# Kernel tuning notes

Measured on AMD Instinct MI355X. Metric: run time of the kernel, lower is better.

## Reference

```python
import jax, jax.numpy as jnp
import numpy as np

B, L, F, H, HDE, E, V, MH, MW, TOUT = 64, 2, 512, 512, 512, 512, 94, 6, 40, 30
V2 = V + 2          # vocab + START/END + NULL slots
T = TOUT + 2        # decode steps
HW = MH * MW
START = V + 1
END = V + 1


def setup_inputs() -> dict:
    key = jax.random.key(0)
    ks = jax.random.split(key, 20)
    s = 0.05  # weight scale for numerical stability
    n = lambda k, shape: jax.random.normal(k, shape, jnp.float32) * s
    d = {}
    d['conv_f'] = jax.random.normal(ks[0], (B, F, MH, MW), jnp.float32)
    d['target'] = jax.random.randint(ks[1], (B, TOUT), 0, 95, dtype=jnp.int32)
    d['w_ih_en'] = n(ks[2], (L, 4 * H, F))
    d['w_hh_en'] = n(ks[3], (L, 4 * H, H))
    d['b_ih_en'] = n(ks[4], (L, 4 * H))
    d['b_hh_en'] = n(ks[5], (L, 4 * H))
    d['embed_w'] = n(ks[6], (V2, H))
    d['w_ih_de'] = n(ks[7], (L, 4 * HDE, H))
    d['w_hh_de'] = n(ks[8], (L, 4 * HDE, HDE))
    d['b_ih_de'] = n(ks[9], (L, 4 * HDE))
    d['b_hh_de'] = n(ks[10], (L, 4 * HDE))
    d['att_wh'] = n(ks[11], (E, HDE))
    d['att_bh'] = n(ks[12], (E,))
    d['att_conv_w'] = n(ks[13], (E, F, 3, 3))
    d['att_conv_b'] = n(ks[14], (E,))
    d['att_wv'] = n(ks[15], (1, E))
    d['att_bv'] = n(ks[16], (1,))
    d['out_w'] = n(ks[17], (V2, HDE + F))
    d['out_b'] = n(ks[18], (V2,))
    return d


def _lstm_cell(x, h, c, wih, whh, bih, bhh):
    # PyTorch gate order: i, f, g, o
    g = x @ wih.T + h @ whh.T + bih + bhh
    i, f, gg, o = jnp.split(g, 4, axis=-1)
    c_new = jax.nn.sigmoid(f) * c + jax.nn.sigmoid(i) * jnp.tanh(gg)
    h_new = jax.nn.sigmoid(o) * jnp.tanh(c_new)
    return h_new, c_new


def _forward(conv_f, target, w_ih_en, w_hh_en, b_ih_en, b_hh_en, embed_w,
             w_ih_de, w_hh_de, b_ih_de, b_hh_de, att_wh, att_bh,
             att_conv_w, att_conv_b, att_wv, att_bv, out_w, out_b):
    # ---- encoder: maxpool over full height, then 2-layer LSTM over width ----
    x_seq = jnp.max(conv_f, axis=2).transpose(2, 0, 1)  # [W, B, F]

    def enc_step(carry, xt):
        h, c = carry
        inp = xt
        hs, cs = [], []
        for l in range(L):
            hl, cl = _lstm_cell(inp, h[l], c[l], w_ih_en[l], w_hh_en[l],
                                b_ih_en[l], b_hh_en[l])
            inp = hl
            hs.append(hl); cs.append(cl)
        return (jnp.stack(hs), jnp.stack(cs)), inp

    z = jnp.zeros((L, B, H), conv_f.dtype)
    _, enc_out = jax.lax.scan(enc_step, (z, z), x_seq)
    holistic = enc_out[-1]  # [B, H]

    # ---- attention: conv_f embedding computed ONCE (invariant across steps) ----
    xe = jax.lax.conv_general_dilated(
        conv_f, att_conv_w, (1, 1), 'SAME',
        dimension_numbers=('NCHW', 'OIHW', 'NCHW')) + att_conv_b[None, :, None, None]
    x_em = xe.reshape(B, E, HW).transpose(0, 2, 1)       # [B, HW, E]
    cf_flat = conv_f.reshape(B, F, HW).transpose(0, 2, 1)  # [B, HW, F]

    # ---- decoder inputs: t=0 holistic, t>=1 embed(gt_with_start[:, t-1]) ----
    gt = jnp.concatenate(
        [jnp.full((B, 1), START, dtype=target.dtype), target], axis=1)  # [B, T-1]
    xs = jnp.concatenate([holistic[None], embed_w[gt.T]], axis=0)  # [T, B, H]

    def dec_step(carry, xt):
        h, c = carry
        inp = xt
        hs, cs = [], []
        for l in range(L):
            hl, cl = _lstm_cell(inp, h[l], c[l], w_ih_de[l], w_hh_de[l],
                                b_ih_de[l], b_hh_de[l])
            inp = hl
            hs.append(hl); cs.append(cl)
        hlast = inp  # [B, HDE]
        g_em = hlast @ att_wh.T + att_bh                    # [B, E]
        feat = jnp.tanh(x_em + g_em[:, None, :])            # [B, HW, E] (dropout=identity)
        e = feat @ att_wv[0] + att_bv[0]                    # [B, HW]
        alpha = jax.nn.softmax(e, axis=-1)
        att = jnp.einsum('bw,bwf->bf', alpha, cf_flat)      # [B, F]
        logits = jnp.concatenate([hlast, att], axis=-1) @ out_w.T + out_b
        scores = jax.nn.log_softmax(logits, axis=-1)        # [B, V2]
        return (jnp.stack(hs), jnp.stack(cs)), scores

    zd = jnp.zeros((B, HDE), conv_f.dtype)
    z0 = jnp.stack([zd] * L)
    _, out_tbv = jax.lax.scan(dec_step, (z0, z0), xs)  # [T, B, V2]
    out = out_tbv.transpose(1, 0, 2)                    # [B, T, V2]

    # ---- build l_target: [0, target..., 0] with first padding 0 -> END ----
    l_target = jnp.zeros((B, T), jnp.int32).at[:, 1:-1].set(target)
    j = jnp.argmax(l_target[:, 1:] == 0, axis=1) + 1  # first zero at col>=1 (always exists)
    l_target = l_target.at[jnp.arange(B), j].set(END)

    # ---- masked NLL loss ----
    lt = l_target.reshape(-1)
    nll = -out.reshape(-1, V2)[jnp.arange(B * T), lt]
    mask = (lt != 0).astype(out.dtype)
    return jnp.sum(nll * mask) / jnp.sum(mask)


def reference(conv_f, target, w_ih_en, w_hh_en, b_ih_en, b_hh_en, embed_w,
              w_ih_de, w_hh_de, b_ih_de, b_hh_de, att_wh, att_bh,
              att_conv_w, att_conv_b, att_wv, att_bv, out_w, out_b):
    return _forward(conv_f, target, w_ih_en, w_hh_en, b_ih_en, b_hh_en, embed_w,
                    w_ih_de, w_hh_de, b_ih_de, b_hh_de, att_wh, att_bh,
                    att_conv_w, att_conv_b, att_wv, att_bv, out_w, out_b)
```

## Files before the change

kernel.cpp:

```cpp
#include <hip/hip_runtime.h>

typedef __fp16 f16;
typedef __fp16 f16x4 __attribute__((ext_vector_type(4)));
typedef __fp16 f16x8 __attribute__((ext_vector_type(8)));
typedef float  f32x4 __attribute__((ext_vector_type(4)));
typedef unsigned long long ull;

#define DEV static __device__ __forceinline__

DEV f32x4 mfma16(f16x4 a, f16x4 b, f32x4 c) {
  return __builtin_amdgcn_mfma_f32_16x16x16f16(a, b, c, 0, 0, 0);
}
DEV f16x4 lo4(f16x8 v) { return __builtin_shufflevector(v, v, 0, 1, 2, 3); }
DEV f16x4 hi4(f16x8 v) { return __builtin_shufflevector(v, v, 4, 5, 6, 7); }
DEV float sigf(float x) { return 1.f / (1.f + __expf(-x)); }
DEV float tanh_(float x) { float e = __expf(2.f * x); return 1.f - 2.f / (e + 1.f); }

union U8 { float4 f4; float2 f2[2]; };
union H2 { unsigned u; f16 h[2]; };
union H4 { ull u; f16 h[4]; f16x4 v; };

#define HB 32768

DEV ull ldU(const ull* p) {
  return __hip_atomic_load(p, __ATOMIC_RELAXED, __HIP_MEMORY_SCOPE_AGENT);
}
DEV unsigned ldF(const unsigned* p) {
  return __hip_atomic_load(p, __ATOMIC_RELAXED, __HIP_MEMORY_SCOPE_AGENT);
}
DEV void stU32(unsigned* p, unsigned v) {
  __hip_atomic_store(p, v, __ATOMIC_RELAXED, __HIP_MEMORY_SCOPE_AGENT);
}
DEV void stU64(ull* p, ull v) {
  __hip_atomic_store(p, v, __ATOMIC_RELAXED, __HIP_MEMORY_SCOPE_AGENT);
}

DEV void wait8(const unsigned* line, unsigned tgt) {
  if (threadIdx.x < 8)
    while (ldF(line + threadIdx.x * 16) < tgt) {}
  __syncthreads();
}

DEV void signalDone(unsigned* line, int slot) {
  asm volatile("s_waitcnt vmcnt(0)" ::: "memory");
  __syncthreads();
  if (threadIdx.x == 0)
    __hip_atomic_fetch_add(line + slot * 16, 1u, __ATOMIC_RELAXED, __HIP_MEMORY_SCOPE_AGENT);
}

DEV void stageRow(const f16* __restrict__ s, f16* __restrict__ dstRow, int ch) {
  U8 u0, u1;
  u0.f4 = *(const float4*)s;
  u1.f4 = *(const float4*)(s + 8);
  *(float2*)(dstRow +  0 + ch * 4) = u0.f2[0];
  *(float2*)(dstRow + 16 + ch * 4) = u0.f2[1];
  *(float2*)(dstRow + 32 + ch * 4) = u1.f2[0];
  *(float2*)(dstRow + 48 + ch * 4) = u1.f2[1];
}

DEV void stageAu(const ull* __restrict__ srcU, f16 (*A)[64][72], int tid) {
  int row = tid >> 2, ch = tid & 3;
  const ull* s = srcU + row * 128 + ch * 4;
#pragma unroll
  for (int c = 0; c < 8; ++c) {
    ull d0 = ldU(s + c * 16 + 0);
    ull d1 = ldU(s + c * 16 + 1);
    ull d2 = ldU(s + c * 16 + 2);
    ull d3 = ldU(s + c * 16 + 3);
    f16* d = &A[c][row][0];
    *(ull*)(d +  0 + ch * 4) = d0;
    *(ull*)(d + 16 + ch * 4) = d1;
    *(ull*)(d + 32 + ch * 4) = d2;
    *(ull*)(d + 48 + ch * 4) = d3;
  }
}

DEV void kloop32(const f16 (*Wt)[32][72], const f16 (*A)[64][72],
                 int mh, int ns, int m16, int g4, f32x4 acc[2]) {
#pragma unroll
  for (int c = 0; c < 8; ++c) {
#pragma unroll
    for (int half = 0; half < 2; ++half) {
      f16x8 bf = *(const f16x8*)&Wt[c][ns * 16 + m16][g4 * 16 + half * 8];
      f16x4 bl = lo4(bf), bh = hi4(bf);
#pragma unroll
      for (int mt = 0; mt < 2; ++mt) {
        f16x8 af = *(const f16x8*)&A[c][mh * 32 + mt * 16 + m16][g4 * 16 + half * 8];
        acc[mt] = mfma16(lo4(af), bl, acc[mt]);
        acc[mt] = mfma16(hi4(af), bh, acc[mt]);
      }
// ... 51 lines not shown
        } else {
          float2 z = make_float2(0.f, 0.f);
          *(float2*)&At[t][ 0] = z; *(float2*)&At[t][ 8] = z;
          *(float2*)&At[t][16] = z; *(float2*)&At[t][24] = z;
          *(float2*)&At[t][ 4] = z; *(float2*)&At[t][12] = z;
          *(float2*)&At[t][20] = z; *(float2*)&At[t][28] = z;
        }
      }
      {
        int n = t >> 1, ch = t & 1;
        const f16* s = wc9 + (size_t)(eb + n) * 4608 + kr * 512 + f0 + ch * 16;
        U8 u0, u1;
        u0.f4 = *(const float4*)s; u1.f4 = *(const float4*)(s + 8);
        *(float2*)&Bt[n][ 0 + ch * 4] = u0.f2[0];
        *(float2*)&Bt[n][ 8 + ch * 4] = u0.f2[1];
        *(float2*)&Bt[n][16 + ch * 4] = u1.f2[0];
        *(float2*)&Bt[n][24 + ch * 4] = u1.f2[1];
      }
      __syncthreads();
      f16x8 b0 = *(const f16x8*)&Bt[w * 32 + m16][g4 * 8];
      f16x8 b1v = *(const f16x8*)&Bt[w * 32 + 16 + m16][g4 * 8];
      f16x4 b0l = lo4(b0), b0h = hi4(b0), b1l = lo4(b1v), b1h = hi4(b1v);
#pragma unroll
      for (int mt = 0; mt < 15; ++mt) {
        f16x8 af = *(const f16x8*)&At[mt * 16 + m16][g4 * 8];
        f16x4 al = lo4(af), ah = hi4(af);
        acc[mt][0] = mfma16(al, b0l, acc[mt][0]);
        acc[mt][1] = mfma16(al, b1l, acc[mt][1]);
        acc[mt][0] = mfma16(ah, b0h, acc[mt][0]);
        acc[mt][1] = mfma16(ah, b1h, acc[mt][1]);
      }
    }
  }
#pragma unroll
  for (int nt = 0; nt < 2; ++nt) {
    int e = eb + w * 32 + nt * 16 + m16;
    float bias = cb[e];
#pragma unroll
    for (int mt = 0; mt < 15; ++mt)
#pragma unroll
      for (int r = 0; r < 4; ++r) {
        int p = mt * 16 + g4 * 4 + r;
        xemH[((size_t)(b * 240 + p)) * 512 + e] = (f16)(acc[mt][nt][r] + bias);
      }
  }
}


__global__ void k_convW(const float* __restrict__ s0, const float* __restrict__ s1,
                        const float* __restrict__ s2, const float* __restrict__ s3,
                        f16* __restrict__ d0, f16* __restrict__ d1,
                        f16* __restrict__ d2, f16* __restrict__ d3) {
  int i = blockIdx.x * 256 + threadIdx.x;
  int sel = i >> 19, j = i & 524287;
  const float* s = sel == 0 ? s0 : sel == 1 ? s1 : sel == 2 ? s2 : s3;
  f16* d = sel == 0 ? d0 : sel == 1 ? d1 : sel == 2 ? d2 : d3;
  float4 v = ((const float4*)s)[j];
  f16x4 o = { (f16)v.x, (f16)v.y, (f16)v.z, (f16)v.w };
  *(f16x4*)(d + (size_t)j * 4) = o;
}

__global__ void k_convS(const float* __restrict__ awhS, const float* __restrict__ embS,
                        const float* __restrict__ outwS,
                        f16* __restrict__ awhD, f16* __restrict__ embD,
                        f16* __restrict__ outwD) {
  int i = blockIdx.x * 256 + threadIdx.x;
  const float* s; f16* d; int j;
  if (i < 65536) { s = awhS; d = awhD; j = i; }
  else if (i < 65536 + 12288) { s = embS; d = embD; j = i - 65536; }
  else if (i < 65536 + 12288 + 24576) { s = outwS; d = outwD; j = i - 65536 - 12288; }
  else return;
  float4 v = ((const float4*)s)[j];
  f16x4 o = { (f16)v.x, (f16)v.y, (f16)v.z, (f16)v.w };
  *(f16x4*)(d + (size_t)j * 4) = o;
}

__global__ __launch_bounds__(256) void k_wc9(const float* __restrict__ src, f16* __restrict__ dst) {
// ... 18 lines not shown
    float4 v = ((const float4*)src)[i];
    int fl = i / 60, pc = (i % 60) * 4;
    sT[fl][pc] = v.x; sT[fl][pc + 1] = v.y; sT[fl][pc + 2] = v.z; sT[fl][pc + 3] = v.w;
  }
  __syncthreads();
  if (tid < 240) {
    int p = tid;
    f16* drow = cfT + ((size_t)b * 240 + p) * 512 + f0;
#pragma unroll
    for (int j = 0; j < 8; ++j) {
      f16x8 o;
#pragma unroll
      for (int k = 0; k < 8; ++k) o[k] = (f16)sT[j * 8 + k][p];
      *(f16x8*)(drow + j * 8) = o;
    }
  }
  {
    int fl = tid >> 2, wq = tid & 3;
#pragma unroll
    for (int wi = 0; wi < 10; ++wi) {
      int w = wq * 10 + wi;
      float m = sT[fl][w];
#pragma unroll
      for (int h = 1; h < 6; ++h) m = fmaxf(m, sT[fl][h * 40 + w]);
      xseq[((size_t)w * 64 + b) * 512 + f0 + fl] = (f16)m;
    }
  }
}

__global__ void k_zero(unsigned* p0, unsigned* p1, unsigned* p2,
                       unsigned* p3, unsigned* p4, unsigned* p5) {
  int i = blockIdx.x * 256 + threadIdx.x;
  int sel = i >> 14, j = i & 16383;
  unsigned* p = sel == 0 ? p0 : sel == 1 ? p1 : sel == 2 ? p2 :
                sel == 3 ? p3 : sel == 4 ? p4 : p5;
  p[j] = 0;
}

__global__ __launch_bounds__(256) void k_gemmX(
    const f16* __restrict__ A, const f16* __restrict__ W,
    const float* __restrict__ b1, const float* __restrict__ b2,
    f16* __restrict__ C)
{
  __shared__ f16 At[64][72];
  __shared__ f16 Bt[64][72];
  const int t = threadIdx.x, lane = t & 63, g = t >> 6;
  f32x4 acc[4] = {};
  const int m16 = lane & 15, g4 = lane >> 4;
  const size_t arow0 = (size_t)blockIdx.x * 64;

  for (int k0 = 0; k0 < 512; k0 += 64) {
    __syncthreads();
    { int row = t >> 2, ch = t & 3;
      stageRow(A + (arow0 + row) * 512 + k0 + ch * 16, &At[row][0], ch); }
    { int row = t >> 2, ch = t & 3;
      stageRow(W + ((size_t)blockIdx.y * 64 + row) * 512 + k0 + ch * 16, &Bt[row][0], ch); }
    __syncthreads();
#pragma unroll
    for (int half = 0; half < 2; ++half) {
      f16x8 bf = *(const f16x8*)&Bt[g * 16 + m16][g4 * 16 + half * 8];
      f16x4 bl = lo4(bf), bh = hi4(bf);
#pragma unroll
      for (int mt = 0; mt < 4; ++mt) {
        f16x8 af = *(const f16x8*)&At[mt * 16 + m16][g4 * 16 + half * 8];
        acc[mt] = mfma16(lo4(af), bl, acc[mt]);
        acc[mt] = mfma16(hi4(af), bh, acc[mt]);
      }
    }
// ... 21 lines not shown
  const size_t arow0 = (size_t)tt * 64;
  const int row = t >> 2, ch = t & 3;
  const f16* rowSrc;
  if (tt == 0) rowSrc = x_t0 + (size_t)row * 512;
  else if (tt == 1) rowSrc = emb + (size_t)95 * 512;
  else { int tok = tgt[row * 30 + tt - 2]; rowSrc = emb + (size_t)tok * 512; }

  for (int k0 = 0; k0 < 512; k0 += 64) {
    __syncthreads();
    stageRow(rowSrc + k0 + ch * 16, &At[row][0], ch);
    stageRow(W + ((size_t)blockIdx.y * 64 + row) * 512 + k0 + ch * 16, &Bt[row][0], ch);
    __syncthreads();
#pragma unroll
    for (int half = 0; half < 2; ++half) {
      f16x8 bf = *(const f16x8*)&Bt[g * 16 + m16][g4 * 16 + half * 8];
      f16x4 bl = lo4(bf), bh = hi4(bf);
#pragma unroll
      for (int mt = 0; mt < 4; ++mt) {
        f16x8 af = *(const f16x8*)&At[mt * 16 + m16][g4 * 16 + half * 8];
        acc[mt] = mfma16(lo4(af), bl, acc[mt]);
        acc[mt] = mfma16(hi4(af), bh, acc[mt]);
      }
    }
  }
  int e = blockIdx.y * 64 + g * 16 + m16;
  float bias = b1[e] + b2[e];
#pragma unroll
  for (int mt = 0; mt < 4; ++mt)
#pragma unroll
    for (int r = 0; r < 4; ++r)
      C[(arow0 + mt * 16 + g4 * 4 + r) * 2048 + e] = (f16)(acc[mt][r] + bias);
}

__global__ __launch_bounds__(256) void k_gemmG(
    const f16* __restrict__ A, const f16* __restrict__ W,
    const float* __restrict__ b1, f16* __restrict__ C)
{
  __shared__ f16 At[64][72];
  __shared__ f16 Bt[64][72];
  const int t = threadIdx.x, lane = t & 63, g = t >> 6;
  f32x4 acc[4] = {};
  const int m16 = lane & 15, g4 = lane >> 4;
  const size_t arow0 = (size_t)blockIdx.x * 64;

  for (int k0 = 0; k0 < 512; k0 += 64) {
    __syncthreads();
    { int row = t >> 2, ch = t & 3;
      stageRow(A + (arow0 + row) * 512 + k0 + ch * 16, &At[row][0], ch); }
    { int row = t >> 2, ch = t & 3;
      stageRow(W + ((size_t)blockIdx.y * 64 + row) * 512 + k0 + ch * 16, &Bt[row][0], ch); }
    __syncthreads();
#pragma unroll
    for (int half = 0; half < 2; ++half) {
      f16x8 bf = *(const f16x8*)&Bt[g * 16 + m16][g4 * 16 + half * 8];
      f16x4 bl = lo4(bf), bh = hi4(bf);
#pragma unroll
      for (int mt = 0; mt < 4; ++mt) {
        f16x8 af = *(const f16x8*)&At[mt * 16 + m16][g4 * 16 + half * 8];
        acc[mt] = mfma16(lo4(af), bl, acc[mt]);
        acc[mt] = mfma16(hi4(af), bh, acc[mt]);
      }
    }
  }
  int e = blockIdx.y * 64 + g * 16 + m16;
  float bias = b1[e];
#pragma unroll
  for (int mt = 0; mt < 4; ++mt)
#pragma unroll
    for (int r = 0; r < 4; ++r)
      C[(arow0 + mt * 16 + g4 * 4 + r) * 512 + e] = (f16)(acc[mt][r] + bias);
}

__global__ __launch_bounds__(256, 1) void k_lstm(
    int T,
    const f16* __restrict__ G0, const f16* __restrict__ whh0,
    const f16* __restrict__ wih1, const f16* __restrict__ whh1,
    const float* __restrict__ bih1, const float* __restrict__ bhh1,
    f16* __restrict__ h0seq, f16* __restrict__ h1seq,
    unsigned* __restrict__ cnt,
    const f16* __restrict__ cfT, const f16* __restrict__ wc9,
    const float* __restrict__ cb, f16* __restrict__ xemH, int convBase)
{
  __shared__ __align__(16) char smem[147456];
  const int tid = threadIdx.x, lane = tid & 63, w = tid >> 6;
  const int m16 = lane & 15, g4 = lane >> 4;
  const int bid = blockIdx.x;

  if (bid >= 96) {
    convTile(smem, convBase + bid - 96, cfT, wc9, cb, xemH);
    return;
  }

  if (bid < 32) {
    f16 (*sW)[64][72] = (f16(*)[64][72])smem;
    f16 (*sA)[64][72] = (f16(*)[64][72])(smem + 73728);
    float* sG = (float*)(smem + 73728);
    const int utile = bid;
    { int r = tid >> 2, ch = tid & 3;
      int grow = (r >> 4) * 512 + utile * 16 + (r & 15);
      for (int c = 0; c < 8; ++c)
        stageRow(whh0 + (size_t)grow * 512 + c * 64 + ch * 16, &sW[c][r][0], ch);
    }
    const int pb = tid >> 2, uq = tid & 3;
    float cst[4] = {0.f, 0.f, 0.f, 0.f};
    for (int t = 0; t < T; ++t) {
      if (t > 0) wait8(cnt + (size_t)(t - 1) * 128, 4);
      const f16* gpp = G0 + (size_t)(t * 64 + pb) * 2048 + utile * 16 + uq * 4;
      H4 gI, gF, gG, gO;
      gI.v = *(const f16x4*)(gpp);
      gF.v = *(const f16x4*)(gpp + 512);
      gG.v = *(const f16x4*)(gpp + 1024);
      gO.v = *(const f16x4*)(gpp + 1536);
      stageAu((const ull*)h0seq + (size_t)t * 8192, sA, tid);
      __syncthreads();
      f32x4 acc[4] = {};
      kloop64((const f16*)sW, sA, w, m16, g4, acc);
      __syncthreads();
#pragma unroll
      for (int mt = 0; mt < 4; ++mt)
#pragma unroll
        for (int r = 0; r < 4; ++r)
          sG[((size_t)w * 64 + mt * 16 + g4 * 4 + r) * 17 + m16] = acc[mt][r];
      __syncthreads();
      {
        H4 outp;
#pragma unroll
        for (int j = 0; j < 4; ++j) {
          int u = uq * 4 + j;
          float gi = sG[(0 * 64 + pb) * 17 + u] + (float)gI.h[j];
          float gf = sG[(1 * 64 + pb) * 17 + u] + (float)gF.h[j];
          float gg = sG[(2 * 64 + pb) * 17 + u] + (float)gG.h[j];
          float go = sG[(3 * 64 + pb) * 17 + u] + (float)gO.h[j];
          float cn = sigf(gf) * cst[j] + sigf(gi) * tanh_(gg);
          float hn = sigf(go) * tanh_(cn);
          cst[j] = cn;
          outp.h[j] = (f16)hn;
        }
        stU64((ull*)h0seq + (size_t)(t + 1) * 8192 + pb * 128 + utile * 4 + uq, outp.u);
      }
      signalDone(cnt + (size_t)t * 128, bid & 7);
    }
  } else {
    f16 (*sW2)[8][32][72] = (f16(*)[8][32][72])smem;
    f16 (*sA)[64][72] = (f16(*)[64][72])(smem + 73728);
    float* sG = (float*)(smem + 73728);
    const int utile = bid - 32;
    const int mh = w >> 1, ns = w & 1;
    { int mat = tid >> 7;
      int r = (tid >> 2) & 31, ch = tid & 3;
      int grow = (r >> 3) * 512 + utile * 8 + (r & 7);
      const f16* Wsrc = (mat == 0) ? wih1 : whh1;
      for (int c = 0; c < 8; ++c)
        stageRow(Wsrc + (size_t)grow * 512 + c * 64 + ch * 16, &sW2[mat][c][r][0], ch);
    }
    const int pb = tid >> 2, pup = tid & 3;
    float badd[4][2];
#pragma unroll
    for (int g = 0; g < 4; ++g)
#pragma unroll
      for (int j = 0; j < 2; ++j) {
        int rr = g * 512 + utile * 8 + pup * 2 + j;
        badd[g][j] = bih1[rr] + bhh1[rr];
      }
    float cst[2] = {0.f, 0.f};
    unsigned* line1 = cnt + (size_t)T * 128;
    for (int t = 0; t < T; ++t) {
      wait8(cnt + (size_t)t * 128, 4);
      stageAu((const ull*)h0seq + (size_t)(t + 1) * 8192, sA, tid);
      if (t > 0) wait8(line1 + (size_t)(t - 1) * 128, 8);
      else       __syncthreads();
      ull rg[8][4];
      { const ull* s1p = (const ull*)h1seq + (size_t)t * 8192 + (tid >> 2) * 128 + (tid & 3) * 4;
#pragma unroll
        for (int c = 0; c < 8; ++c)
#pragma unroll
// ... 13 lines not shown
        }
      }
      __syncthreads();
      kloop32(sW2[1], sA, mh, ns, m16, g4, acc);
      __syncthreads();
      { int nl = ns * 16 + m16;
#pragma unroll
        for (int mt = 0; mt < 2; ++mt)
#pragma unroll
          for (int r = 0; r < 4; ++r) {
            int b = mh * 32 + mt * 16 + g4 * 4 + r;
            sG[((nl >> 3) * 64 + b) * 9 + (nl & 7)] = acc[mt][r];
          }
      }
      __syncthreads();
      {
        H2 outp;
#pragma unroll
        for (int j = 0; j < 2; ++j) {
          int u = pup * 2 + j;
          float gi = sG[(0 * 64 + pb) * 9 + u] + badd[0][j];
          float gf = sG[(1 * 64 + pb) * 9 + u] + badd[1][j];
          float gg = sG[(2 * 64 + pb) * 9 + u] + badd[2][j];
          float go = sG[(3 * 64 + pb) * 9 + u] + badd[3][j];
          float cn = sigf(gf) * cst[j] + sigf(gi) * tanh_(gg);
          float hn = sigf(go) * tanh_(cn);
          cst[j] = cn;
          outp.h[j] = (f16)hn;
        }
        stU32((unsigned*)h1seq + (size_t)(t + 1) * 16384 + pb * 256 + utile * 4 + pup, outp.u);
      }
      signalDone(line1 + (size_t)t * 128, bid & 7);
    }
  }
}


__global__ __launch_bounds__(256) void k_scoreAll(
    const f16* __restrict__ xemH, const f16* __restrict__ gAll,
    const float* __restrict__ wv, float* __restrict__ esc)
{
  __shared__ f16 sX[20][512];
  const int tid = threadIdx.x, lane = tid & 63, w = tid >> 6;
  const int tile = blockIdx.x, b = blockIdx.y;
  for (int i = tid; i < 20 * 64; i += 256) {
    int row = i >> 6, seg = i & 63;
    *(f16x8*)&sX[row][seg * 8] =
        *(const f16x8*)(xemH + ((size_t)(b * 240 + tile * 20 + row)) * 512 + seg * 8);
  }
  float w8[8];
  { const float4* wp = (const float4*)(wv + lane * 8);
    float4 wa = wp[0], wb = wp[1];
    w8[0] = wa.x; w8[1] = wa.y; w8[2] = wa.z; w8[3] = wa.w;
    w8[4] = wb.x; w8[5] = wb.y; w8[6] = wb.z; w8[7] = wb.w; }
  __syncthreads();
  for (int t = 0; t < 32; ++t) {
    f16x8 gv = *(const f16x8*)(gAll + ((size_t)(t * 64 + b)) * 512 + lane * 8);
    float g8[8];
#pragma unroll
    for (int j = 0; j < 8; ++j) g8[j] = (float)gv[j];
#pragma unroll
    for (int i = 0; i < 5; ++i) {
      int rr = i * 4 + w;
      f16x8 xv = *(const f16x8*)&sX[rr][lane * 8];
      float s = 0.f;
#pragma unroll
      for (int j = 0; j < 8; ++j) s += tanh_((float)xv[j] + g8[j]) * w8[j];
#pragma unroll
      for (int m = 32; m; m >>= 1) s += __shfl_xor(s, m);
      if (lane == 0) esc[((size_t)(t * 64 + b)) * 240 + tile * 20 + rr] = s;
    }
  }
}

__global__ __launch_bounds__(256) void k_smctx(
    const float* __restrict__ esc, const f16* __restrict__ cfT,
    const f16* __restrict__ h1seq, f16* __restrict__ ctx)
{
  __shared__ float aAl[8][240];
  const int tid = threadIdx.x, lane = tid & 63, w = tid >> 6;
  const int tq = blockIdx.x, b = blockIdx.y;
  for (int half = 0; half < 2; ++half) {
    int tt = w + half * 4;
    int t = tq * 8 + tt;
    const float* er = esc + ((size_t)(t * 64 + b)) * 240;
    float v[4];
    float mx = -1e30f;
#pragma unroll
    for (int q = 0; q < 4; ++q) {
      int p = lane + q * 64;
      v[q] = (p < 240) ? er[p] : -1e30f;
      mx = fmaxf(mx, v[q]);
    }
#pragma unroll
    for (int m = 32; m; m >>= 1) mx = fmaxf(mx, __shfl_xor(mx, m));
    float sum = 0.f;
#pragma unroll
    for (int q = 0; q < 4; ++q) { v[q] = __expf(v[q] - mx); sum += v[q]; }
#pragma unroll
    for (int m = 32; m; m >>= 1) sum += __shfl_xor(sum, m);
    float inv = 1.f / sum;
#pragma unroll
    for (int q = 0; q < 4; ++q) {
      int p = lane + q * 64;
      if (p < 240) aAl[tt][p] = v[q] * inv;
    }
  }
  __syncthreads();
  float acc[8][2] = {};
  const f16* cb = cfT + (size_t)b * 240 * 512;
  for (int p = 0; p < 240; ++p) {
    H2 cw; cw.u = *(const unsigned*)(cb + (size_t)p * 512 + tid * 2);
    float c0 = (float)cw.h[0], c1 = (float)cw.h[1];
#pragma unroll
    for (int tt = 0; tt < 8; ++tt) {
      float a = aAl[tt][p];
      acc[tt][0] += a * c0;
      acc[tt][1] += a * c1;
    }
  }
#pragma unroll
  for (int tt = 0; tt < 8; ++tt) {
    int t = tq * 8 + tt;
    size_t r = (size_t)(t * 64 + b);
    H2 o; o.h[0] = (f16)acc[tt][0]; o.h[1] = (f16)acc[tt][1];
    *(unsigned*)(ctx + r * 1024 + 512 + tid * 2) = o.u;
    *(unsigned*)(ctx + r * 1024 + tid * 2) =
        *(const unsigned*)(h1seq + (size_t)(t + 1) * HB + b * 512 + tid * 2);
  }
}

__global__ __launch_bounds__(256) void k_gemmL(
    const f16* __restrict__ A, const f16* __restrict__ W,
    const float* __restrict__ bias, float* __restrict__ C)
{
  __shared__ f16 At[64][72];
  __shared__ f16 Bt[64][72];
  const int t = threadIdx.x, lane = t & 63, g = t >> 6;
  f32x4 acc[4] = {};
  const int m16 = lane & 15, g4 = lane >> 4;
  const size_t arow0 = (size_t)blockIdx.x * 64;

  for (int k0 = 0; k0 < 1024; k0 += 64) {
    __syncthreads();
    { int row = t >> 2, ch = t & 3;
      stageRow(A + (arow0 + row) * 1024 + k0 + ch * 16, &At[row][0], ch); }
    { int row = t >> 2, ch = t & 3;
      stageRow(W + ((size_t)(blockIdx.y * 64 + row)) * 1024 + k0 + ch * 16, &Bt[row][0], ch); }
    __syncthreads();
#pragma unroll
    for (int half = 0; half < 2; ++half) {
      f16x8 bf = *(const f16x8*)&Bt[g * 16 + m16][g4 * 16 + half * 8];
      f16x4 bl = lo4(bf), bh = hi4(bf);
#pragma unroll
      for (int mt = 0; mt < 4; ++mt) {
        f16x8 af = *(const f16x8*)&At[mt * 16 + m16][g4 * 16 + half * 8];
        acc[mt] = mfma16(lo4(af), bl, acc[mt]);
        acc[mt] = mfma16(hi4(af), bh, acc[mt]);
      }
    }
  }
  int e = blockIdx.y * 64 + g * 16 + m16;
  if (e < 96) {
    float be = bias[e];
#pragma unroll
    for (int mt = 0; mt < 4; ++mt)
#pragma unroll
      for (int r = 0; r < 4; ++r)
        C[(arow0 + mt * 16 + g4 * 4 + r) * 96 + e] = acc[mt][r] + be;
  }
}

__global__ void k_nllloss(const float* __restrict__ lgt, const int* __restrict__ target,
                          float* __restrict__ out) {
  __shared__ int ltg[2048];
  __shared__ float sa[256], sb[256];
  int tid = threadIdx.x;
  if (tid < 64) {
    int b = tid;
    int row[32];
    row[0] = 0;
    for (int t = 1; t <= 30; ++t) row[t] = target[b * 30 + t - 1];
    row[31] = 0;
    int j = 1;
    while (row[j] != 0) ++j;
    row[j] = 95;
    for (int t = 0; t < 32; ++t) ltg[b * 32 + t] = row[t];
  }
  __syncthreads();
  float a = 0.f, m = 0.f;
  for (int r = tid; r < 2048; r += 256) {
    int t = r >> 6, b = r & 63;
    int tok = ltg[b * 32 + t];
    if (tok != 0) {
      const float* row = lgt + (size_t)r * 96;
      float mx = -1e30f;
      for (int j = 0; j < 96; ++j) mx = fmaxf(mx, row[j]);
      float s = 0.f;
      for (int j = 0; j < 96; ++j) s += __expf(row[j] - mx);
      a += mx + __logf(s) - row[tok];
      m += 1.f;
    }
  }
  sa[tid] = a; sb[tid] = m; __syncthreads();
  for (int s = 128; s; s >>= 1) { if (tid < s) { sa[tid] += sa[tid + s]; sb[tid] += sb[tid + s]; } __syncthreads(); }
  if (tid == 0) out[0] = sa[0] / sb[0];
}


extern "C" void kernel_launch(void* const* d_in, const int* in_sizes, int n_in,
                              void* d_out, int out_size, void* d_ws, size_t ws_size,
                              hipStream_t stream) {
  (void)in_sizes; (void)n_in; (void)out_size; (void)ws_size;
  const float* conv_f = (const float*)d_in[0];
  const int*   target = (const int*)d_in[1];
  const float* wih_en = (const float*)d_in[2];
  const float* whh_en = (const float*)d_in[3];
  const float* bih_en = (const float*)d_in[4];
  const float* bhh_en = (const float*)d_in[5];
  const float* embed  = (const float*)d_in[6];
  const float* wih_de = (const float*)d_in[7];
  const float* whh_de = (const float*)d_in[8];
  const float* bih_de = (const float*)d_in[9];
  const float* bhh_de = (const float*)d_in[10];
  const float* att_wh = (const float*)d_in[11];
  const float* att_bh = (const float*)d_in[12];
  const float* att_cw = (const float*)d_in[13];
  const float* att_cb = (const float*)d_in[14];
  const float* att_wv = (const float*)d_in[15];
  const float* out_w  = (const float*)d_in[17];
  const float* out_b  = (const float*)d_in[18];
  float* out = (float*)d_out;

  size_t o = 0;
  char* base = (char*)d_ws;
  auto take = [&](size_t bytes) -> void* {
    void* p = base + o;
    o += (bytes + 255) & ~(size_t)255;
    return p;
  };
  const size_t WSZ = (size_t)2048 * 512;
  f16* wihEn = (f16*)take(2 * WSZ * 2);
  f16* whhEn = (f16*)take(2 * WSZ * 2);
  f16* wihDe = (f16*)take(2 * WSZ * 2);
  f16* whhDe = (f16*)take(2 * WSZ * 2);
  f16* awh   = (f16*)take((size_t)512 * 512 * 2);
  f16* emb   = (f16*)take((size_t)96 * 512 * 2);
  f16* wc9   = (f16*)take((size_t)512 * 4608 * 2);
  f16* cfT   = (f16*)take((size_t)64 * 240 * 512 * 2);
  f16* xseq  = (f16*)take((size_t)40 * 64 * 512 * 2);
  f16* xemH  = (f16*)take((size_t)64 * 240 * 512 * 2);
  f16* outwH = (f16*)take((size_t)128 * 1024 * 2);
  f16* X0en  = (f16*)take((size_t)2560 * 2048 * 2);
  f16* X0de  = (f16*)take((size_t)2048 * 2048 * 2);
  f16* h0seqE = (f16*)take((size_t)41 * HB * 2);
  f16* h1seqE = (f16*)take((size_t)41 * HB * 2);
  f16* h0seqD = (f16*)take((size_t)33 * HB * 2);
  f16* h1seqD = (f16*)take((size_t)33 * HB * 2);
  f16* gAll   = (f16*)take((size_t)2048 * 512 * 2);
  unsigned* cntE = (unsigned*)take(65536);
  unsigned* cntD = (unsigned*)take(65536);
  float* escAll = (float*)X0en;
  float* lgtAll = (float*)((char*)X0en + 4194304);
  f16*   ctxAll = X0de;

  k_convW<<<8192, 256, 0, stream>>>(wih_en, whh_en, wih_de, whh_de,
                                    wihEn, whhEn, wihDe, whhDe);
  k_convS<<<400, 256, 0, stream>>>(att_wh, embed, out_w, awh, emb, outwH);
  k_wc9<<<512, 256, 0, stream>>>(att_cw, wc9);
  k_cfmx<<<dim3(8, 64), 256, 0, stream>>>(conv_f, cfT, xseq);
  k_zero<<<384, 256, 0, stream>>>((unsigned*)h0seqE, (unsigned*)h1seqE,
                                  (unsigned*)h0seqD, (unsigned*)h1seqD, cntE, cntD);

  k_gemmX<<<dim3(40, 32), 256, 0, stream>>>(xseq, wihEn, bih_en, bhh_en, X0en);
  k_lstm<<<224, 256, 0, stream>>>(40, X0en, whhEn, wihEn + WSZ, whhEn + WSZ,
                                  bih_en + 2048, bhh_en + 2048, h0seqE, h1seqE, cntE,
                                  cfT, wc9, att_cb, xemH, 0);

  k_gemmXd<<<dim3(32, 32), 256, 0, stream>>>(h1seqE + (size_t)40 * HB, emb, target,
                                             wihDe, bih_de, bhh_de, X0de);
  k_lstm<<<224, 256, 0, stream>>>(32, X0de, whhDe, wihDe + WSZ, whhDe + WSZ,
                                  bih_de + 2048, bhh_de + 2048, h0seqD, h1seqD, cntD,
                                  cfT, wc9, att_cb, xemH, 128);

  k_gemmG<<<dim3(32, 8), 256, 0, stream>>>(h1seqD + HB, awh, att_bh, gAll);
  k_scoreAll<<<dim3(12, 64), 256, 0, stream>>>(xemH, gAll, att_wv, escAll);
  k_smctx<<<dim3(4, 64), 256, 0, stream>>>(escAll, cfT, h1seqD, ctxAll);
  k_gemmL<<<dim3(32, 2), 256, 0, stream>>>(ctxAll, outwH, out_b, lgtAll);
  k_nllloss<<<1, 256, 0, stream>>>(lgtAll, target, out);
}
```

Measured before the change: 856.4 us.

## Fuse attention, logits and NLL tail into persistent LSTM kernel with flag pipelining

The post-decoder stages (attention-query GEMM, score computation, softmax-context, logit GEMM, per-token NLL) move into the idle conv blocks of the decoder LSTM kernel. They are chained by counter flags so they overlap with the recurrence instead of running as separate launches. The embedding part of the decoder input GEMM is computed by extra blocks during the encoder LSTM, leaving only the t=0 row for k_gemmXd. The conv tile output is staged through LDS for coalesced atomic stores. The cost is more spin-waiting, atomic-load traffic and scratch buffers, and a risk of deadlock if the blocks are not all co-resident.

```diff
diff --git a/kernel.cpp b/kernel.cpp
--- a/kernel.cpp
+++ b/kernel.cpp
@@ -19,6 +19,7 @@
 union U8 { float4 f4; float2 f2[2]; };
 union H2 { unsigned u; f16 h[2]; };
 union H4 { ull u; f16 h[4]; f16x4 v; };
+union U32F { unsigned u; float f; };
 
 #define HB 32768
 
@@ -35,11 +36,12 @@
   __hip_atomic_store(p, v, __ATOMIC_RELAXED, __HIP_MEMORY_SCOPE_AGENT);
 }
 
-DEV void wait8(const unsigned* line, unsigned tgt) {
-  if (threadIdx.x < 8)
+DEV void waitN(const unsigned* line, int n, unsigned tgt) {
+  if ((int)threadIdx.x < n)
     while (ldF(line + threadIdx.x * 16) < tgt) {}
   __syncthreads();
 }
+DEV void wait8(const unsigned* line, unsigned tgt) { waitN(line, 8, tgt); }
 
 DEV void signalDone(unsigned* line, int slot) {
   asm volatile("s_waitcnt vmcnt(0)" ::: "memory");
@@ -56,6 +58,14 @@
   *(float2*)(dstRow + 16 + ch * 4) = u0.f2[1];
   *(float2*)(dstRow + 32 + ch * 4) = u1.f2[0];
   *(float2*)(dstRow + 48 + ch * 4) = u1.f2[1];
+}
+
+DEV void stageAp(const f16* __restrict__ rowSrc, f16 (*A)[64][72], int tid) {
+  int ch = tid & 3;
+  const f16* s = rowSrc + ch * 16;
+#pragma unroll
+  for (int c = 0; c < 8; ++c)
+    stageRow(s + c * 64, &A[c][tid >> 2][0], ch);
 }
 
 DEV void stageAu(const ull* __restrict__ srcU, f16 (*A)[64][72], int tid) {
@@ -173,6 +183,8 @@
       }
     }
   }
+  f16 (*sC)[132] = (f16(*)[132])smem;
+  __syncthreads();
 #pragma unroll
   for (int nt = 0; nt < 2; ++nt) {
     int e = eb + w * 32 + nt * 16 + m16;
@@ -180,10 +192,16 @@
 #pragma unroll
     for (int mt = 0; mt < 15; ++mt)
 #pragma unroll
-      for (int r = 0; r < 4; ++r) {
-        int p = mt * 16 + g4 * 4 + r;
-        xemH[((size_t)(b * 240 + p)) * 512 + e] = (f16)(acc[mt][nt][r] + bias);
-      }
+      for (int r = 0; r < 4; ++r)
+        sC[mt * 16 + g4 * 4 + r][w * 32 + nt * 16 + m16] = (f16)(acc[mt][nt][r] + bias);
+  }
+  __syncthreads();
+#pragma unroll
+  for (int k = 0; k < 30; ++k) {
+    int id = t + k * 256;
+    int row = id >> 5, chk = id & 31;
+    H4 pk; pk.v = *(const f16x4*)&sC[row][chk * 4];
+    stU64((ull*)xemH + (size_t)(b * 240 + row) * 128 + (eb >> 2) + chk, pk.u);
   }
 }
 
@@ -268,8 +286,13 @@
                        unsigned* p3, unsigned* p4, unsigned* p5) {
   int i = blockIdx.x * 256 + threadIdx.x;
   int sel = i >> 14, j = i & 16383;
-  unsigned* p = sel == 0 ? p0 : sel == 1 ? p1 : sel == 2 ? p2 :
-                sel == 3 ? p3 : sel == 4 ? p4 : p5;
+  unsigned* p;
+  if (sel == 0) p = p0;
+  else if (sel == 1) p = p1;
+  else if (sel == 2) p = p2;
+  else if (sel == 3) p = p3;
+  else if (sel == 4) p = p4;
+  else p = p5 + (size_t)(sel - 5) * 16384;
   p[j] = 0;
 }
 
@@ -357,64 +380,27 @@
       C[(arow0 + mt * 16 + g4 * 4 + r) * 2048 + e] = (f16)(acc[mt][r] + bias);
 }
 
-__global__ __launch_bounds__(256) void k_gemmG(
-    const f16* __restrict__ A, const f16* __restrict__ W,
-    const float* __restrict__ b1, f16* __restrict__ C)
-{
-  __shared__ f16 At[64][72];
-  __shared__ f16 Bt[64][72];
-  const int t = threadIdx.x, lane = t & 63, g = t >> 6;
-  f32x4 acc[4] = {};
-  const int m16 = lane & 15, g4 = lane >> 4;
-  const size_t arow0 = (size_t)blockIdx.x * 64;
-
-  for (int k0 = 0; k0 < 512; k0 += 64) {
-    __syncthreads();
-    { int row = t >> 2, ch = t & 3;
-      stageRow(A + (arow0 + row) * 512 + k0 + ch * 16, &At[row][0], ch); }
-    { int row = t >> 2, ch = t & 3;
-      stageRow(W + ((size_t)blockIdx.y * 64 + row) * 512 + k0 + ch * 16, &Bt[row][0], ch); }
-    __syncthreads();
-#pragma unroll
-    for (int half = 0; half < 2; ++half) {
-      f16x8 bf = *(const f16x8*)&Bt[g * 16 + m16][g4 * 16 + half * 8];
-      f16x4 bl = lo4(bf), bh = hi4(bf);
-#pragma unroll
-      for (int mt = 0; mt < 4; ++mt) {
-        f16x8 af = *(const f16x8*)&At[mt * 16 + m16][g4 * 16 + half * 8];
-        acc[mt] = mfma16(lo4(af), bl, acc[mt]);
-        acc[mt] = mfma16(hi4(af), bh, acc[mt]);
-      }
-    }
-  }
-  int e = blockIdx.y * 64 + g * 16 + m16;
-  float bias = b1[e];
-#pragma unroll
-  for (int mt = 0; mt < 4; ++mt)
-#pragma unroll
-    for (int r = 0; r < 4; ++r)
-      C[(arow0 + mt * 16 + g4 * 4 + r) * 512 + e] = (f16)(acc[mt][r] + bias);
-}
-
 __global__ __launch_bounds__(256, 1) void k_lstm(
-    int T,
+    int T, int mode,
     const f16* __restrict__ G0, const f16* __restrict__ whh0,
     const f16* __restrict__ wih1, const f16* __restrict__ whh1,
     const float* __restrict__ bih1, const float* __restrict__ bhh1,
     f16* __restrict__ h0seq, f16* __restrict__ h1seq,
     unsigned* __restrict__ cnt,
     const f16* __restrict__ cfT, const f16* __restrict__ wc9,
-    const float* __restrict__ cb, f16* __restrict__ xemH, int convBase)
+    const float* __restrict__ cb, f16* __restrict__ xemH, int convBase,
+    f16* __restrict__ X0de, const f16* __restrict__ wihD0,
+    const float* __restrict__ bihD0, const float* __restrict__ bhhD0,
+    const f16* __restrict__ emb, const int* __restrict__ tgt,
+    const f16* __restrict__ awh, const float* __restrict__ gbias, f16* __restrict__ gAll,
+    const float* __restrict__ wv, const f16* __restrict__ outwH, const float* __restrict__ outb,
+    float* __restrict__ escAll, f16* __restrict__ ctxAll, float* __restrict__ lgtAll,
+    float* __restrict__ nllb)
 {
   __shared__ __align__(16) char smem[147456];
   const int tid = threadIdx.x, lane = tid & 63, w = tid >> 6;
   const int m16 = lane & 15, g4 = lane >> 4;
   const int bid = blockIdx.x;
-
-  if (bid >= 96) {
-    convTile(smem, convBase + bid - 96, cfT, wc9, cb, xemH);
-    return;
-  }
 
   if (bid < 32) {
     f16 (*sW)[64][72] = (f16(*)[64][72])smem;
@@ -465,7 +451,7 @@
       }
       signalDone(cnt + (size_t)t * 128, bid & 7);
     }
-  } else {
+  } else if (bid < 96) {
     f16 (*sW2)[8][32][72] = (f16(*)[8][32][72])smem;
     f16 (*sA)[64][72] = (f16(*)[64][72])(smem + 73728);
     float* sG = (float*)(smem + 73728);
@@ -545,175 +531,268 @@
       }
       signalDone(line1 + (size_t)t * 128, bid & 7);
     }
-  }
-}
-
-
-__global__ __launch_bounds__(256) void k_scoreAll(
-    const f16* __restrict__ xemH, const f16* __restrict__ gAll,
-    const float* __restrict__ wv, float* __restrict__ esc)
-{
-  __shared__ f16 sX[20][512];
-  const int tid = threadIdx.x, lane = tid & 63, w = tid >> 6;
-  const int tile = blockIdx.x, b = blockIdx.y;
-  for (int i = tid; i < 20 * 64; i += 256) {
-    int row = i >> 6, seg = i & 63;
-    *(f16x8*)&sX[row][seg * 8] =
-        *(const f16x8*)(xemH + ((size_t)(b * 240 + tile * 20 + row)) * 512 + seg * 8);
-  }
-  float w8[8];
-  { const float4* wp = (const float4*)(wv + lane * 8);
-    float4 wa = wp[0], wb = wp[1];
-    w8[0] = wa.x; w8[1] = wa.y; w8[2] = wa.z; w8[3] = wa.w;
-    w8[4] = wb.x; w8[5] = wb.y; w8[6] = wb.z; w8[7] = wb.w; }
-  __syncthreads();
-  for (int t = 0; t < 32; ++t) {
-    f16x8 gv = *(const f16x8*)(gAll + ((size_t)(t * 64 + b)) * 512 + lane * 8);
-    float g8[8];
-#pragma unroll
-    for (int j = 0; j < 8; ++j) g8[j] = (float)gv[j];
-#pragma unroll
-    for (int i = 0; i < 5; ++i) {
-      int rr = i * 4 + w;
-      f16x8 xv = *(const f16x8*)&sX[rr][lane * 8];
-      float s = 0.f;
-#pragma unroll
-      for (int j = 0; j < 8; ++j) s += tanh_((float)xv[j] + g8[j]) * w8[j];
-#pragma unroll
-      for (int m = 32; m; m >>= 1) s += __shfl_xor(s, m);
-      if (lane == 0) esc[((size_t)(t * 64 + b)) * 240 + tile * 20 + rr] = s;
-    }
-  }
-}
-
-__global__ __launch_bounds__(256) void k_smctx(
-    const float* __restrict__ esc, const f16* __restrict__ cfT,
-    const f16* __restrict__ h1seq, f16* __restrict__ ctx)
-{
-  __shared__ float aAl[8][240];
-  const int tid = threadIdx.x, lane = tid & 63, w = tid >> 6;
-  const int tq = blockIdx.x, b = blockIdx.y;
-  for (int half = 0; half < 2; ++half) {
-    int tt = w + half * 4;
-    int t = tq * 8 + tt;
-    const float* er = esc + ((size_t)(t * 64 + b)) * 240;
-    float v[4];
-    float mx = -1e30f;
-#pragma unroll
-    for (int q = 0; q < 4; ++q) {
-      int p = lane + q * 64;
-      v[q] = (p < 240) ? er[p] : -1e30f;
-      mx = fmaxf(mx, v[q]);
-    }
-#pragma unroll
-    for (int m = 32; m; m >>= 1) mx = fmaxf(mx, __shfl_xor(mx, m));
-    float sum = 0.f;
-#pragma unroll
-    for (int q = 0; q < 4; ++q) { v[q] = __expf(v[q] - mx); sum += v[q]; }
-#pragma unroll
-    for (int m = 32; m; m >>= 1) sum += __shfl_xor(sum, m);
-    float inv = 1.f / sum;
-#pragma unroll
-    for (int q = 0; q < 4; ++q) {
-      int p = lane + q * 64;
-      if (p < 240) aAl[tt][p] = v[q] * inv;
-    }
-  }
-  __syncthreads();
-  float acc[8][2] = {};
-  const f16* cb = cfT + (size_t)b * 240 * 512;
-  for (int p = 0; p < 240; ++p) {
-    H2 cw; cw.u = *(const unsigned*)(cb + (size_t)p * 512 + tid * 2);
-    float c0 = (float)cw.h[0], c1 = (float)cw.h[1];
-#pragma unroll
-    for (int tt = 0; tt < 8; ++tt) {
-      float a = aAl[tt][p];
-      acc[tt][0] += a * c0;
-      acc[tt][1] += a * c1;
-    }
-  }
-#pragma unroll
-  for (int tt = 0; tt < 8; ++tt) {
-    int t = tq * 8 + tt;
-    size_t r = (size_t)(t * 64 + b);
-    H2 o; o.h[0] = (f16)acc[tt][0]; o.h[1] = (f16)acc[tt][1];
-    *(unsigned*)(ctx + r * 1024 + 512 + tid * 2) = o.u;
-    *(unsigned*)(ctx + r * 1024 + tid * 2) =
-        *(const unsigned*)(h1seq + (size_t)(t + 1) * HB + b * 512 + tid * 2);
-  }
-}
-
-__global__ __launch_bounds__(256) void k_gemmL(
-    const f16* __restrict__ A, const f16* __restrict__ W,
-    const float* __restrict__ bias, float* __restrict__ C)
-{
-  __shared__ f16 At[64][72];
-  __shared__ f16 Bt[64][72];
-  const int t = threadIdx.x, lane = t & 63, g = t >> 6;
-  f32x4 acc[4] = {};
-  const int m16 = lane & 15, g4 = lane >> 4;
-  const size_t arow0 = (size_t)blockIdx.x * 64;
-
-  for (int k0 = 0; k0 < 1024; k0 += 64) {
+  } else if (mode == 0 && bid >= 224) {
+    const int rid = bid - 224;
+    f16 (*sW)[64][72] = (f16(*)[64][72])smem;
+    f16 (*sA)[64][72] = (f16(*)[64][72])(smem + 73728);
+    { int r = tid >> 2, ch = tid & 3;
+      for (int c = 0; c < 8; ++c)
+        stageRow(wihD0 + (size_t)(rid * 64 + r) * 512 + c * 64 + ch * 16, &sW[c][r][0], ch);
+    }
+    const int e = rid * 64 + w * 16 + m16;
+    const float bias_e = bihD0[e] + bhhD0[e];
+    const int arow = tid >> 2;
     __syncthreads();
-    { int row = t >> 2, ch = t & 3;
-      stageRow(A + (arow0 + row) * 1024 + k0 + ch * 16, &At[row][0], ch); }
-    { int row = t >> 2, ch = t & 3;
-      stageRow(W + ((size_t)(blockIdx.y * 64 + row)) * 1024 + k0 + ch * 16, &Bt[row][0], ch); }
-    __syncthreads();
-#pragma unroll
-    for (int half = 0; half < 2; ++half) {
-      f16x8 bf = *(const f16x8*)&Bt[g * 16 + m16][g4 * 16 + half * 8];
-      f16x4 bl = lo4(bf), bh = hi4(bf);
-#pragma unroll
-      for (int mt = 0; mt < 4; ++mt) {
-        f16x8 af = *(const f16x8*)&At[mt * 16 + m16][g4 * 16 + half * 8];
-        acc[mt] = mfma16(lo4(af), bl, acc[mt]);
-        acc[mt] = mfma16(hi4(af), bh, acc[mt]);
-      }
-    }
-  }
-  int e = blockIdx.y * 64 + g * 16 + m16;
-  if (e < 96) {
-    float be = bias[e];
-#pragma unroll
-    for (int mt = 0; mt < 4; ++mt)
-#pragma unroll
-      for (int r = 0; r < 4; ++r)
-        C[(arow0 + mt * 16 + g4 * 4 + r) * 96 + e] = acc[mt][r] + be;
-  }
-}
-
-__global__ void k_nllloss(const float* __restrict__ lgt, const int* __restrict__ target,
-                          float* __restrict__ out) {
-  __shared__ int ltg[2048];
+    for (int tt = 1; tt < 32; ++tt) {
+      const f16* rowSrc = (tt == 1) ? emb + (size_t)95 * 512
+                                    : emb + (size_t)tgt[arow * 30 + tt - 2] * 512;
+      stageAp(rowSrc, sA, tid);
+      __syncthreads();
+      f32x4 acc[4] = {};
+      kloop64((const f16*)sW, sA, w, m16, g4, acc);
+      __syncthreads();
+#pragma unroll
+      for (int mt = 0; mt < 4; ++mt)
+#pragma unroll
+        for (int r = 0; r < 4; ++r)
+          X0de[((size_t)tt * 64 + mt * 16 + g4 * 4 + r) * 2048 + e] = (f16)(acc[mt][r] + bias_e);
+      __syncthreads();
+    }
+  } else if (mode == 0) {
+    convTile(smem, convBase + bid - 96, cfT, wc9, cb, xemH);
+  } else {
+    const int c = bid - 96;
+    convTile(smem, convBase + c, cfT, wc9, cb, xemH);
+    signalDone(cnt + 8192, c & 7);
+    unsigned* GL = cnt + 8320;
+    unsigned* SL = cnt + 12416;
+    unsigned* CL = cnt + 45184;
+    unsigned* LL = cnt + 45696;
+    unsigned* line1 = cnt + (size_t)T * 128;
+
+    {
+      const int n = c & 7;
+      f16* sWg = (f16*)smem;
+      f16 (*sA)[64][72] = (f16(*)[64][72])(smem + 73728);
+      f16 (*sC)[72] = (f16(*)[72])(smem + 73728 + 36864);
+      __syncthreads();
+      { int r = tid >> 2, ch = tid & 3;
+        for (int cc = 0; cc < 8; ++cc)
+          stageRow(awh + (size_t)(n * 64 + r) * 512 + cc * 64 + ch * 16,
+                   sWg + ((size_t)(cc * 64 + r)) * 72, ch);
+      }
+      const int e = n * 64 + w * 16 + m16;
+      const float gb = gbias[e];
+      __syncthreads();
+      for (int rep = 0; rep < 2; ++rep) {
+        int t = (c >> 3) + rep * 16;
+        wait8(line1 + (size_t)t * 128, 8);
+        stageAu((const ull*)h1seq + (size_t)(t + 1) * 8192, sA, tid);
+        __syncthreads();
+        f32x4 acc[4] = {};
+        kloop64(sWg, sA, w, m16, g4, acc);
+        __syncthreads();
+#pragma unroll
+        for (int mt = 0; mt < 4; ++mt)
+#pragma unroll
+          for (int r = 0; r < 4; ++r)
+            sC[mt * 16 + g4 * 4 + r][w * 16 + m16] = (f16)(acc[mt][r] + gb);
+        __syncthreads();
+#pragma unroll
+        for (int k = 0; k < 4; ++k) {
+          int id = tid + k * 256;
+          int row = id >> 4, chk = id & 15;
+          H4 pk; pk.v = *(const f16x4*)&sC[row][chk * 4];
+          stU64((ull*)gAll + (size_t)(t * 64 + row) * 128 + n * 16 + chk, pk.u);
+        }
+        signalDone(GL + (size_t)t * 128, n);
+        __syncthreads();
+      }
+    }
+    wait8(cnt + 8192, 16);
+    {
+      float w8[8];
+      { const float4* wp = (const float4*)(wv + lane * 8);
+        float4 wa = wp[0], wb2 = wp[1];
+        w8[0] = wa.x; w8[1] = wa.y; w8[2] = wa.z; w8[3] = wa.w;
+        w8[4] = wb2.x; w8[5] = wb2.y; w8[6] = wb2.z; w8[7] = wb2.w; }
+      float* sE = (float*)smem;
+      for (int id = c; id < 2048; id += 128) {
+        int t = id >> 6, b = id & 63;
+        waitN(GL + (size_t)t * 128, 8, 1);
+        const ull* gp = (const ull*)gAll + (size_t)(t * 64 + b) * 128 + lane * 2;
+        H4 ga, gb4; ga.u = ldU(gp); gb4.u = ldU(gp + 1);
+        float g8[8];
+#pragma unroll
+        for (int j = 0; j < 4; ++j) { g8[j] = (float)ga.h[j]; g8[4 + j] = (float)gb4.h[j]; }
+        for (int r = w; r < 240; r += 4) {
+          const ull* xp = (const ull*)xemH + (size_t)(b * 240 + r) * 128 + lane * 2;
+          H4 xa, xb; xa.u = ldU(xp); xb.u = ldU(xp + 1);
+          float s = 0.f;
+#pragma unroll
+          for (int j = 0; j < 4; ++j) s += tanh_((float)xa.h[j] + g8[j]) * w8[j];
+#pragma unroll
+          for (int j = 0; j < 4; ++j) s += tanh_((float)xb.h[j] + g8[4 + j]) * w8[4 + j];
+#pragma unroll
+          for (int m = 32; m; m >>= 1) s += __shfl_xor(s, m);
+          if (lane == 0) sE[r] = s;
+        }
+        __syncthreads();
+        if (tid < 240) {
+          U32F u; u.f = sE[tid];
+          stU32((unsigned*)escAll + (size_t)(t * 64 + b) * 240 + tid, u.u);
+        }
+        signalDone(SL + (size_t)((t >> 3) * 64 + b) * 128, t & 7);
+        __syncthreads();
+      }
+    }
+    {
+      float* aAl = (float*)smem;
+      for (int id = c; id < 256; id += 128) {
+        int tq = id >> 6, b = id & 63;
+        waitN(SL + (size_t)id * 128, 8, 1);
+        for (int half = 0; half < 2; ++half) {
+          int tt = w + half * 4;
+          int t = tq * 8 + tt;
+          const unsigned* er = (const unsigned*)escAll + (size_t)(t * 64 + b) * 240;
+          float v[4]; float mx = -1e30f;
+#pragma unroll
+          for (int q = 0; q < 4; ++q) {
+            int p = lane + q * 64;
+            if (p < 240) { U32F u; u.u = ldF(er + p); v[q] = u.f; } else v[q] = -1e30f;
+            mx = fmaxf(mx, v[q]);
+          }
+#pragma unroll
+          for (int m = 32; m; m >>= 1) mx = fmaxf(mx, __shfl_xor(mx, m));
+          float sum = 0.f;
+#pragma unroll
+          for (int q = 0; q < 4; ++q) { v[q] = __expf(v[q] - mx); sum += v[q]; }
+#pragma unroll
+          for (int m = 32; m; m >>= 1) sum += __shfl_xor(sum, m);
+          float inv = 1.f / sum;
+#pragma unroll
+          for (int q = 0; q < 4; ++q) {
+            int p = lane + q * 64;
+            if (p < 240) aAl[tt * 240 + p] = v[q] * inv;
+          }
+        }
+        __syncthreads();
+        float acc2[8][2] = {};
+        const f16* cbp = cfT + (size_t)b * 240 * 512;
+        for (int p = 0; p < 240; ++p) {
+          H2 cw; cw.u = *(const unsigned*)(cbp + (size_t)p * 512 + tid * 2);
+          float c0 = (float)cw.h[0], c1 = (float)cw.h[1];
+#pragma unroll
+          for (int tt = 0; tt < 8; ++tt) {
+            float a = aAl[tt * 240 + p];
+            acc2[tt][0] += a * c0;
+            acc2[tt][1] += a * c1;
+          }
+        }
+#pragma unroll
+        for (int tt = 0; tt < 8; ++tt) {
+          int t = tq * 8 + tt;
+          size_t r = (size_t)(t * 64 + b);
+          H2 o; o.h[0] = (f16)acc2[tt][0]; o.h[1] = (f16)acc2[tt][1];
+          stU32((unsigned*)ctxAll + r * 512 + 256 + tid, o.u);
+          unsigned hv = ldF((const unsigned*)h1seq + (size_t)(t + 1) * 16384 + b * 256 + tid);
+          stU32((unsigned*)ctxAll + r * 512 + tid, hv);
+        }
+        signalDone(CL + (size_t)tq * 128, b & 7);
+        __syncthreads();
+      }
+    }
+    if (c < 64) {
+      int t = c >> 1, n2 = c & 1;
+      waitN(CL + (size_t)(t >> 3) * 128, 8, 8);
+      f16 (*At)[72] = (f16(*)[72])smem;
+      f16 (*Bt)[72] = (f16(*)[72])(smem + 16384);
+      f32x4 acc[4] = {};
+      for (int k0 = 0; k0 < 1024; k0 += 64) {
+        __syncthreads();
+        { int row = tid >> 2, ch = tid & 3;
+          const ull* rb = (const ull*)ctxAll + (size_t)(t * 64 + row) * 256 + (k0 >> 2) + ch * 4;
+          ull d0 = ldU(rb), d1 = ldU(rb + 1), d2 = ldU(rb + 2), d3 = ldU(rb + 3);
+          f16* dr = &At[row][0];
+          *(ull*)(dr +  0 + ch * 4) = d0;
+          *(ull*)(dr + 16 + ch * 4) = d1;
+          *(ull*)(dr + 32 + ch * 4) = d2;
+          *(ull*)(dr + 48 + ch * 4) = d3;
+        }
+        { int row = tid >> 2, ch = tid & 3;
+          stageRow(outwH + (size_t)(n2 * 64 + row) * 1024 + k0 + ch * 16, &Bt[row][0], ch); }
+        __syncthreads();
+#pragma unroll
+        for (int half = 0; half < 2; ++half) {
+          f16x8 bf = *(const f16x8*)&Bt[w * 16 + m16][g4 * 16 + half * 8];
+          f16x4 bl = lo4(bf), bh = hi4(bf);
+#pragma unroll
+          for (int mt = 0; mt < 4; ++mt) {
+            f16x8 af = *(const f16x8*)&At[mt * 16 + m16][g4 * 16 + half * 8];
+            acc[mt] = mfma16(lo4(af), bl, acc[mt]);
+            acc[mt] = mfma16(hi4(af), bh, acc[mt]);
+          }
+        }
+      }
+      int e = n2 * 64 + w * 16 + m16;
+      if (e < 96) {
+        float be = outb[e];
+#pragma unroll
+        for (int mt = 0; mt < 4; ++mt)
+#pragma unroll
+          for (int r = 0; r < 4; ++r) {
+            U32F u; u.f = acc[mt][r] + be;
+            stU32((unsigned*)lgtAll + (size_t)(t * 64 + mt * 16 + g4 * 4 + r) * 96 + e, u.u);
+          }
+      }
+      signalDone(LL + (size_t)t * 128, n2);
+    }
+    if (c >= 64 && c < 96) {
+      int t = c - 64;
+      waitN(LL + (size_t)t * 128, 2, 1);
+      if (tid < 64) {
+        int b = tid;
+        int jj = 31;
+        for (int q = 1; q <= 30; ++q)
+          if (tgt[b * 30 + q - 1] == 0) { jj = q; break; }
+        int tok = (t == 0 || t == 31) ? 0 : tgt[b * 30 + t - 1];
+        if (t == jj) tok = 95;
+        float val = 0.f;
+        if (tok != 0) {
+          const unsigned* lp = (const unsigned*)lgtAll + (size_t)(t * 64 + b) * 96;
+          float mx = -1e30f;
+          for (int j = 0; j < 96; ++j) { U32F u; u.u = ldF(lp + j); mx = fmaxf(mx, u.f); }
+          float s = 0.f;
+          for (int j = 0; j < 96; ++j) { U32F u; u.u = ldF(lp + j); s += __expf(u.f - mx); }
+          U32F ut; ut.u = ldF(lp + tok);
+          val = mx + __logf(s) - ut.f;
+        }
+        U32F o; o.f = val;
+        stU32((unsigned*)nllb + t * 64 + b, o.u);
+      }
+    }
+  }
+}
+
+__global__ void k_loss(const float* __restrict__ nllb, const int* __restrict__ tgt,
+                       float* __restrict__ out) {
   __shared__ float sa[256], sb[256];
   int tid = threadIdx.x;
+  float a = 0.f, m = 0.f;
+  for (int i = tid; i < 2048; i += 256) a += nllb[i];
   if (tid < 64) {
     int b = tid;
-    int row[32];
-    row[0] = 0;
-    for (int t = 1; t <= 30; ++t) row[t] = target[b * 30 + t - 1];
-    row[31] = 0;
-    int j = 1;
-    while (row[j] != 0) ++j;
-    row[j] = 95;
-    for (int t = 0; t < 32; ++t) ltg[b * 32 + t] = row[t];
-  }
-  __syncthreads();
-  float a = 0.f, m = 0.f;
-  for (int r = tid; r < 2048; r += 256) {
-    int t = r >> 6, b = r & 63;
-    int tok = ltg[b * 32 + t];
-    if (tok != 0) {
-      const float* row = lgt + (size_t)r * 96;
-      float mx = -1e30f;
-      for (int j = 0; j < 96; ++j) mx = fmaxf(mx, row[j]);
-      float s = 0.f;
-      for (int j = 0; j < 96; ++j) s += __expf(row[j] - mx);
-      a += mx + __logf(s) - row[tok];
-      m += 1.f;
-    }
+    int jj = 31;
+    for (int q = 1; q <= 30; ++q)
+      if (tgt[b * 30 + q - 1] == 0) { jj = q; break; }
+    int cnt = 0;
+    for (int t = 1; t <= 30; ++t) {
+      int v = tgt[b * 30 + t - 1];
+      if (t == jj) v = 95;
+      if (v != 0) ++cnt;
+    }
+    if (jj == 31) ++cnt;
+    m = (float)cnt;
   }
   sa[tid] = a; sb[tid] = m; __syncthreads();
   for (int s = 128; s; s >>= 1) { if (tid < s) { sa[tid] += sa[tid + s]; sb[tid] += sb[tid + s]; } __syncthreads(); }
@@ -771,34 +850,37 @@
   f16* h0seqD = (f16*)take((size_t)33 * HB * 2);
   f16* h1seqD = (f16*)take((size_t)33 * HB * 2);
   f16* gAll   = (f16*)take((size_t)2048 * 512 * 2);
+  float* nllb = (float*)take((size_t)2048 * 4);
   unsigned* cntE = (unsigned*)take(65536);
-  unsigned* cntD = (unsigned*)take(65536);
+  unsigned* cntD = (unsigned*)take(262144);
   float* escAll = (float*)X0en;
   float* lgtAll = (float*)((char*)X0en + 4194304);
-  f16*   ctxAll = X0de;
+  f16*   ctxAll = (f16*)((char*)X0en + 6291456);
 
   k_convW<<<8192, 256, 0, stream>>>(wih_en, whh_en, wih_de, whh_de,
                                     wihEn, whhEn, wihDe, whhDe);
   k_convS<<<400, 256, 0, stream>>>(att_wh, embed, out_w, awh, emb, outwH);
   k_wc9<<<512, 256, 0, stream>>>(att_cw, wc9);
   k_cfmx<<<dim3(8, 64), 256, 0, stream>>>(conv_f, cfT, xseq);
-  k_zero<<<384, 256, 0, stream>>>((unsigned*)h0seqE, (unsigned*)h1seqE,
+  k_zero<<<576, 256, 0, stream>>>((unsigned*)h0seqE, (unsigned*)h1seqE,
                                   (unsigned*)h0seqD, (unsigned*)h1seqD, cntE, cntD);
 
   k_gemmX<<<dim3(40, 32), 256, 0, stream>>>(xseq, wihEn, bih_en, bhh_en, X0en);
-  k_lstm<<<224, 256, 0, stream>>>(40, X0en, whhEn, wihEn + WSZ, whhEn + WSZ,
+  k_lstm<<<256, 256, 0, stream>>>(40, 0, X0en, whhEn, wihEn + WSZ, whhEn + WSZ,
                                   bih_en + 2048, bhh_en + 2048, h0seqE, h1seqE, cntE,
-                                  cfT, wc9, att_cb, xemH, 0);
-
-  k_gemmXd<<<dim3(32, 32), 256, 0, stream>>>(h1seqE + (size_t)40 * HB, emb, target,
-                                             wihDe, bih_de, bhh_de, X0de);
-  k_lstm<<<224, 256, 0, stream>>>(32, X0de, whhDe, wihDe + WSZ, whhDe + WSZ,
+                                  cfT, wc9, att_cb, xemH, 0,
+                                  X0de, wihDe, bih_de, bhh_de, emb, target,
+                                  awh, att_bh, gAll, att_wv, outwH, out_b,
+                                  escAll, ctxAll, lgtAll, nllb);
+
+  k_gemmXd<<<dim3(1, 32), 256, 0, stream>>>(h1seqE + (size_t)40 * HB, emb, target,
+                                            wihDe, bih_de, bhh_de, X0de);
+  k_lstm<<<224, 256, 0, stream>>>(32, 1, X0de, whhDe, wihDe + WSZ, whhDe + WSZ,
                                   bih_de + 2048, bhh_de + 2048, h0seqD, h1seqD, cntD,
-                                  cfT, wc9, att_cb, xemH, 128);
-
-  k_gemmG<<<dim3(32, 8), 256, 0, stream>>>(h1seqD + HB, awh, att_bh, gAll);
-  k_scoreAll<<<dim3(12, 64), 256, 0, stream>>>(xemH, gAll, att_wv, escAll);
-  k_smctx<<<dim3(4, 64), 256, 0, stream>>>(escAll, cfT, h1seqD, ctxAll);
-  k_gemmL<<<dim3(32, 2), 256, 0, stream>>>(ctxAll, outwH, out_b, lgtAll);
-  k_nllloss<<<1, 256, 0, stream>>>(lgtAll, target, out);
-}
+                                  cfT, wc9, att_cb, xemH, 128,
+                                  X0de, wihDe, bih_de, bhh_de, emb, target,
+                                  awh, att_bh, gAll, att_wv, outwH, out_b,
+                                  escAll, ctxAll, lgtAll, nllb);
+
+  k_loss<<<1, 256, 0, stream>>>(nllb, target, out);
+}
```

Result: slower. 1.246 ms (+45.5%).
